# Performance work log

Hardware: AMD Instinct MI355X
Metric: run time of the kernel (lower is better)

Reference implementation:

```python
import jax, jax.numpy as jnp
import numpy as np

B, H, S, DK, DV = 2, 16, 2048, 64, 64

def setup_inputs() -> dict:
    key = jax.random.key(0)
    k1, k2, k3 = jax.random.split(key, 3)
    Q = jax.random.normal(k1, (B, H, S, DK), dtype=jnp.float32)
    K = jax.random.normal(k2, (B, H, S, DK), dtype=jnp.float32)
    V = jax.random.normal(k3, (B, H, S, DV), dtype=jnp.float32)
    mask = jnp.zeros((1, 1, S, S), dtype=jnp.float32)  # additive mask, broadcastable
    return {"Q": Q, "K": K, "V": V, "mask": mask}

def reference(Q, K, V, mask):
    d_k = Q.shape[-1]
    scale = 1.0 / jnp.sqrt(jnp.asarray(d_k, dtype=Q.dtype))
    # [..., q, k] = Q @ K^T / sqrt(d_k) + mask (additive)
    logits = jnp.einsum('bhqd,bhkd->bhqk', Q, K) * scale + mask
    attn = jax.nn.softmax(logits, axis=-1)
    return jnp.einsum('bhqk,bhkv->bhqv', attn, V)
```

## Files before the change

kernel.cpp:

```cpp
#include <hip/hip_runtime.h>


constexpr int Bn = 2, Hn = 16, Sn = 2048, Dn = 64;
constexpr int QB = 128;
constexpr int KVB = 64;
constexpr int NIT = Sn / KVB;
constexpr float SCALE = 0.125f;
constexpr float DEFER_THR = 8.0f;

typedef __attribute__((ext_vector_type(8))) short bf16x8;
typedef __attribute__((ext_vector_type(4))) float f32x4;
typedef __attribute__((ext_vector_type(16))) float f32x16;

union FragU { bf16x8 v; unsigned u[4]; };

__device__ __forceinline__ unsigned cvt_pk(float lo, float hi) {
  unsigned r;
  asm("v_cvt_pk_bf16_f32 %0, %1, %2" : "=v"(r) : "v"(lo), "v"(hi));
  return r;
}

__global__ __launch_bounds__(256, 2) void sdpa_fa3(
    const float* __restrict__ Q, const float* __restrict__ K,
    const float* __restrict__ V, const float* __restrict__ M,
    float* __restrict__ Out) {
  __shared__ unsigned short Kt[2][64 * 64];
  __shared__ unsigned short Vt[2][64 * 64];

  const int tid = threadIdx.x;
  const int lane = tid & 63;
  const int wave = tid >> 6;
  const int l31 = lane & 31;
  const int hi = lane >> 5;
  const int l7 = lane & 7;

  int bid = blockIdx.x;
  bid = (bid & 7) * ((int)gridDim.x >> 3) + (bid >> 3);
  const int head = bid >> 4;
  const int qblk = bid & 15;
  const int qrow = qblk * QB + wave * 32 + l31;

  const float* __restrict__ Qh = Q + (size_t)head * Sn * Dn;
  const float* __restrict__ Kh = K + (size_t)head * Sn * Dn;
  const float* __restrict__ Vh = V + (size_t)head * Sn * Dn;
  float* __restrict__ Oh = Out + (size_t)head * Sn * Dn;
  const float* __restrict__ Mrow = M + (size_t)qrow * Sn;

  FragU qf[4];
#pragma unroll
  for (int kc = 0; kc < 4; ++kc) {
    const float* p = Qh + (size_t)qrow * Dn + kc * 16 + hi * 8;
    f32x4 a = *(const f32x4*)p;
    f32x4 b = *(const f32x4*)(p + 4);
    qf[kc].u[0] = cvt_pk(a[0] * SCALE, a[1] * SCALE);
    qf[kc].u[1] = cvt_pk(a[2] * SCALE, a[3] * SCALE);
    qf[kc].u[2] = cvt_pk(b[0] * SCALE, b[1] * SCALE);
    qf[kc].u[3] = cvt_pk(b[2] * SCALE, b[3] * SCALE);
  }

  f32x16 acc0, acc1;
#pragma unroll
  for (int i = 0; i < 16; ++i) { acc0[i] = 0.f; acc1[i] = 0.f; }
  float m_run = -1e30f, l_run = 0.f;

  const int krow = tid >> 2, kcb = tid & 3;
  const int vk4 = tid >> 4, vcb = tid & 15;

  f32x4 kr[4], vr[4];
  {
    const float* kp = Kh + (size_t)krow * Dn + kcb * 16;
#pragma unroll
    for (int u = 0; u < 4; ++u) kr[u] = *(const f32x4*)(kp + 4 * u);
    const float* vp = Vh + (size_t)(4 * vk4) * Dn + vcb * 4;
#pragma unroll
    for (int r = 0; r < 4; ++r) vr[r] = *(const f32x4*)(vp + (size_t)r * Dn);
#pragma unroll
    for (int b = 0; b < 2; ++b) {
      FragU f;
      f.u[0] = cvt_pk(kr[2 * b][0], kr[2 * b][1]);
      f.u[1] = cvt_pk(kr[2 * b][2], kr[2 * b][3]);
      f.u[2] = cvt_pk(kr[2 * b + 1][0], kr[2 * b + 1][1]);
      f.u[3] = cvt_pk(kr[2 * b + 1][2], kr[2 * b + 1][3]);
      const int pos = (2 * kcb + b) ^ (krow & 7);
      *(bf16x8*)&Kt[0][krow * 64 + pos * 8] = f.v;
    }
#pragma unroll
    for (int j = 0; j < 4; ++j) {
      const int d = 4 * vcb + j;
      unsigned w0 = cvt_pk(vr[0][j], vr[1][j]);
      unsigned w1 = cvt_pk(vr[2][j], vr[3][j]);
      const int pos = (vk4 >> 1) ^ (d & 7);
      unsigned* dst = (unsigned*)&Vt[0][d * 64 + pos * 8 + (vk4 & 1) * 4];
      dst[0] = w0; dst[1] = w1;
    }
  }
  __syncthreads();

  for (int it = 0; it < NIT; ++it) {
    const int kv0 = it * KVB;
    const int cur = it & 1;
    const unsigned short* Kb = Kt[cur];
    const unsigned short* Vb = Vt[cur];

    if (it + 1 < NIT) {
      const float* kp = Kh + (size_t)(kv0 + KVB + krow) * Dn + kcb * 16;
#pragma unroll
      for (int u = 0; u < 4; ++u) kr[u] = *(const f32x4*)(kp + 4 * u);
      const float* vp = Vh + (size_t)(kv0 + KVB + 4 * vk4) * Dn + vcb * 4;
#pragma unroll
      for (int r = 0; r < 4; ++r) vr[r] = *(const f32x4*)(vp + (size_t)r * Dn);
    }

#pragma unroll
    for (int t = 0; t < 2; ++t) {
      f32x4 mk[4];
#pragma unroll
      for (int m = 0; m < 4; ++m)
        mk[m] = *(const f32x4*)(Mrow + kv0 + 32 * t + 8 * m + 4 * hi);

      f32x16 st;
#pragma unroll
      for (int i = 0; i < 16; ++i) st[i] = 0.f;
      __builtin_amdgcn_s_setprio(1);
#pragma unroll
      for (int kc = 0; kc < 4; ++kc) {
        FragU kf;
        kf.v = *(const bf16x8*)&Kb[(32 * t + l31) * 64 + (((2 * kc + hi) ^ l7) * 8)];
        st = __builtin_amdgcn_mfma_f32_32x32x16_bf16(kf.v, qf[kc].v, st, 0, 0, 0);
      }
      __builtin_amdgcn_s_setprio(0);

      float p[16];
#pragma unroll
      for (int m = 0; m < 4; ++m)
#pragma unroll
        for (int e = 0; e < 4; ++e) p[4 * m + e] = st[4 * m + e] + mk[m][e];

      float t8[8];
#pragma unroll
      for (int i = 0; i < 8; ++i) t8[i] = fmaxf(p[2 * i], p[2 * i + 1]);
      float t4a = fmaxf(t8[0], t8[1]), t4b = fmaxf(t8[2], t8[3]);
      float t4c = fmaxf(t8[4], t8[5]), t4d = fmaxf(t8[6], t8[7]);
      float mx = fmaxf(fmaxf(t4a, t4b), fmaxf(t4c, t4d));
      mx = fmaxf(mx, __shfl_xor(mx, 32, 64));

      if (!__all(mx <= m_run + DEFER_THR)) {
        const float mn = fmaxf(m_run, mx);
        const float corr = __expf(m_run - mn);
        m_run = mn;
        l_run *= corr;
#pragma unroll
        for (int i = 0; i < 16; ++i) { acc0[i] *= corr; acc1[i] *= corr; }
      }

      float ps = 0.f;
#pragma unroll
      for (int i = 0; i < 16; ++i) {
        p[i] = __expf(p[i] - m_run);
        ps += p[i];
      }
      ps += __shfl_xor(ps, 32, 64);
      l_run += ps;

      unsigned W[4][2];
#pragma unroll
      for (int m = 0; m < 4; ++m)
#pragma unroll
        for (int s = 0; s < 2; ++s)
          W[m][s] = cvt_pk(p[4 * m + 2 * s], p[4 * m + 2 * s + 1]);

      FragU pf[2];
#pragma unroll
      for (int cc = 0; cc < 2; ++cc)
#pragma unroll
        for (int s = 0; s < 2; ++s) {
          const unsigned a = W[2 * cc][s];
          const unsigned b = W[2 * cc + 1][s];
          const unsigned pa = (unsigned)__shfl_xor((int)a, 32, 64);
          const unsigned pb = (unsigned)__shfl_xor((int)b, 32, 64);
          pf[cc].u[s] = hi ? pb : a;
          pf[cc].u[2 + s] = hi ? b : pa;
        }

      __builtin_amdgcn_s_setprio(1);
#pragma unroll
      for (int cc = 0; cc < 2; ++cc) {
        const int c = 2 * t + cc;
        FragU vf0, vf1;
        vf0.v = *(const bf16x8*)&Vb[(l31) * 64 + (((2 * c + hi) ^ l7) * 8)];
        vf1.v = *(const bf16x8*)&Vb[(32 + l31) * 64 + (((2 * c + hi) ^ l7) * 8)];
        acc0 = __builtin_amdgcn_mfma_f32_32x32x16_bf16(vf0.v, pf[cc].v, acc0, 0, 0, 0);
        acc1 = __builtin_amdgcn_mfma_f32_32x32x16_bf16(vf1.v, pf[cc].v, acc1, 0, 0, 0);
      }
      __builtin_amdgcn_s_setprio(0);
    }

    if (it + 1 < NIT) {
#pragma unroll
      for (int b = 0; b < 2; ++b) {
        FragU f;
        f.u[0] = cvt_pk(kr[2 * b][0], kr[2 * b][1]);
        f.u[1] = cvt_pk(kr[2 * b][2], kr[2 * b][3]);
        f.u[2] = cvt_pk(kr[2 * b + 1][0], kr[2 * b + 1][1]);
        f.u[3] = cvt_pk(kr[2 * b + 1][2], kr[2 * b + 1][3]);
        const int pos = (2 * kcb + b) ^ (krow & 7);
        *(bf16x8*)&Kt[cur ^ 1][krow * 64 + pos * 8] = f.v;
      }
#pragma unroll
      for (int j = 0; j < 4; ++j) {
        const int d = 4 * vcb + j;
        unsigned w0 = cvt_pk(vr[0][j], vr[1][j]);
        unsigned w1 = cvt_pk(vr[2][j], vr[3][j]);
        const int pos = (vk4 >> 1) ^ (d & 7);
        unsigned* dst = (unsigned*)&Vt[cur ^ 1][d * 64 + pos * 8 + (vk4 & 1) * 4];
        dst[0] = w0; dst[1] = w1;
      }
    }
    __syncthreads();
  }

  const float inv = 1.0f / l_run;
#pragma unroll
  for (int m = 0; m < 4; ++m) {
    f32x4 o0, o1;
#pragma unroll
    for (int e = 0; e < 4; ++e) { o0[e] = acc0[4 * m + e] * inv; o1[e] = acc1[4 * m + e] * inv; }
    *(f32x4*)&Oh[(size_t)qrow * Dn + 8 * m + 4 * hi] = o0;
    *(f32x4*)&Oh[(size_t)qrow * Dn + 32 + 8 * m + 4 * hi] = o1;
  }
}

extern "C" void kernel_launch(void* const* d_in, const int* in_sizes, int n_in,
                              void* d_out, int out_size, void* d_ws, size_t ws_size,
                              hipStream_t stream) {
  const float* Q = (const float*)d_in[0];
  const float* K = (const float*)d_in[1];
  const float* V = (const float*)d_in[2];
  const float* M = (const float*)d_in[3];
  float* O = (float*)d_out;
  dim3 grid(Bn * Hn * (Sn / QB));
  sdpa_fa3<<<grid, dim3(256), 0, stream>>>(Q, K, V, M, O);
}
```

Before: 190.7 us.

## Split KV range across two wave groups per block with LDS merge, exp2 softmax

Each block now runs 512 threads, with two groups of four waves each processing half of the KV sequence (split-K style). The partial outputs are merged through LDS at the end using the running max and sum. The tile shrinks to 32 KV rows per iteration. The mask is staged cooperatively into LDS as bf16 pre-scaled by log2e, and the softmax uses raw v_exp_f32 with log2e folded into the Q scale. This is meant to raise parallelism and occupancy and cut the per-lane uncoalesced mask loads. In exchange it doubles the syncthreads count, adds a final LDS reduction, and rounds the mask to bf16, which could lose precision for non-zero masks.

```diff
diff --git a/kernel.cpp b/kernel.cpp
--- a/kernel.cpp
+++ b/kernel.cpp
@@ -3,48 +3,66 @@
 
 constexpr int Bn = 2, Hn = 16, Sn = 2048, Dn = 64;
 constexpr int QB = 128;
-constexpr int KVB = 64;
-constexpr int NIT = Sn / KVB;
-constexpr float SCALE = 0.125f;
+constexpr int KVB = 32;
+constexpr int HALFKV = 1024;
+constexpr int NIT = HALFKV / KVB;
+constexpr float LOG2E = 1.44269504088896f;
+constexpr float QSCALE = 0.125f * LOG2E;
 constexpr float DEFER_THR = 8.0f;
 
 typedef __attribute__((ext_vector_type(8))) short bf16x8;
 typedef __attribute__((ext_vector_type(4))) float f32x4;
 typedef __attribute__((ext_vector_type(16))) float f32x16;
 
-union FragU { bf16x8 v; unsigned u[4]; };
+union FragU { bf16x8 v; unsigned u[4]; unsigned short s[8]; };
+union B64U { unsigned long long q; unsigned short s[4]; };
 
 __device__ __forceinline__ unsigned cvt_pk(float lo, float hi) {
   unsigned r;
   asm("v_cvt_pk_bf16_f32 %0, %1, %2" : "=v"(r) : "v"(lo), "v"(hi));
   return r;
 }
-
-__global__ __launch_bounds__(256, 2) void sdpa_fa3(
+__device__ __forceinline__ float exp2_fast(float x) {
+  float r;
+  asm("v_exp_f32 %0, %1" : "=v"(r) : "v"(x));
+  return r;
+}
+__device__ __forceinline__ float bf2f(unsigned short b) {
+  union { unsigned u; float f; } c;
+  c.u = ((unsigned)b) << 16;
+  return c.f;
+}
+
+__global__ __launch_bounds__(512, 4) void sdpa_fa4(
     const float* __restrict__ Q, const float* __restrict__ K,
     const float* __restrict__ V, const float* __restrict__ M,
     float* __restrict__ Out) {
-  __shared__ unsigned short Kt[2][64 * 64];
-  __shared__ unsigned short Vt[2][64 * 64];
+  __shared__ __align__(16) unsigned short lds[32768];
 
   const int tid = threadIdx.x;
   const int lane = tid & 63;
   const int wave = tid >> 6;
+  const int wq = wave & 3;
+  const int half = tid >> 8;
+  const int htid = tid & 255;
   const int l31 = lane & 31;
   const int hi = lane >> 5;
-  const int l7 = lane & 7;
 
   int bid = blockIdx.x;
   bid = (bid & 7) * ((int)gridDim.x >> 3) + (bid >> 3);
   const int head = bid >> 4;
   const int qblk = bid & 15;
-  const int qrow = qblk * QB + wave * 32 + l31;
+  const int qrow = qblk * QB + wq * 32 + l31;
+  const int kvh = half * HALFKV;
 
   const float* __restrict__ Qh = Q + (size_t)head * Sn * Dn;
   const float* __restrict__ Kh = K + (size_t)head * Sn * Dn;
   const float* __restrict__ Vh = V + (size_t)head * Sn * Dn;
   float* __restrict__ Oh = Out + (size_t)head * Sn * Dn;
-  const float* __restrict__ Mrow = M + (size_t)qrow * Sn;
+
+  unsigned short* Kt = lds + half * 16384;
+  unsigned short* Vt = lds + half * 16384 + 4096;
+  unsigned short* Mt = lds + half * 16384 + 8192;
 
   FragU qf[4];
 #pragma unroll
@@ -52,10 +70,10 @@
     const float* p = Qh + (size_t)qrow * Dn + kc * 16 + hi * 8;
     f32x4 a = *(const f32x4*)p;
     f32x4 b = *(const f32x4*)(p + 4);
-    qf[kc].u[0] = cvt_pk(a[0] * SCALE, a[1] * SCALE);
-    qf[kc].u[1] = cvt_pk(a[2] * SCALE, a[3] * SCALE);
-    qf[kc].u[2] = cvt_pk(b[0] * SCALE, b[1] * SCALE);
-    qf[kc].u[3] = cvt_pk(b[2] * SCALE, b[3] * SCALE);
+    qf[kc].u[0] = cvt_pk(a[0] * QSCALE, a[1] * QSCALE);
+    qf[kc].u[1] = cvt_pk(a[2] * QSCALE, a[3] * QSCALE);
+    qf[kc].u[2] = cvt_pk(b[0] * QSCALE, b[1] * QSCALE);
+    qf[kc].u[3] = cvt_pk(b[2] * QSCALE, b[3] * QSCALE);
   }
 
   f32x16 acc0, acc1;
@@ -63,170 +81,210 @@
   for (int i = 0; i < 16; ++i) { acc0[i] = 0.f; acc1[i] = 0.f; }
   float m_run = -1e30f, l_run = 0.f;
 
-  const int krow = tid >> 2, kcb = tid & 3;
-  const int vk4 = tid >> 4, vcb = tid & 15;
-
-  f32x4 kr[4], vr[4];
+  const int krow = htid >> 3, kcb = htid & 7;
+  const int vd = htid & 63, vkb = htid >> 6;
+  const int mq = htid >> 1, mh = htid & 1;
+
+  f32x4 kr0, kr1;
+  float vrg[8];
+  f32x4 mr[4];
+
   {
-    const float* kp = Kh + (size_t)krow * Dn + kcb * 16;
-#pragma unroll
-    for (int u = 0; u < 4; ++u) kr[u] = *(const f32x4*)(kp + 4 * u);
-    const float* vp = Vh + (size_t)(4 * vk4) * Dn + vcb * 4;
-#pragma unroll
-    for (int r = 0; r < 4; ++r) vr[r] = *(const f32x4*)(vp + (size_t)r * Dn);
-#pragma unroll
-    for (int b = 0; b < 2; ++b) {
+    const float* kp = Kh + (size_t)(kvh + krow) * Dn + kcb * 8;
+    kr0 = *(const f32x4*)kp;
+    kr1 = *(const f32x4*)(kp + 4);
+    const float* vp = Vh + (size_t)(kvh + vkb * 8) * Dn + vd;
+#pragma unroll
+    for (int r = 0; r < 8; ++r) vrg[r] = vp[(size_t)r * Dn];
+    const float* mp = M + (size_t)(qblk * QB + mq) * Sn + kvh + mh * 16;
+#pragma unroll
+    for (int u = 0; u < 4; ++u) mr[u] = *(const f32x4*)(mp + 4 * u);
+
+    FragU f;
+    f.u[0] = cvt_pk(kr0[0], kr0[1]); f.u[1] = cvt_pk(kr0[2], kr0[3]);
+    f.u[2] = cvt_pk(kr1[0], kr1[1]); f.u[3] = cvt_pk(kr1[2], kr1[3]);
+    *(bf16x8*)&Kt[krow * 64 + ((kcb ^ (krow & 7)) * 8)] = f.v;
+    FragU g;
+    g.u[0] = cvt_pk(vrg[0], vrg[1]); g.u[1] = cvt_pk(vrg[2], vrg[3]);
+    g.u[2] = cvt_pk(vrg[4], vrg[5]); g.u[3] = cvt_pk(vrg[6], vrg[7]);
+    *(bf16x8*)&Vt[vd * 32 + ((vkb ^ ((vd >> 2) & 3)) * 8)] = g.v;
+    FragU h0, h1;
+    h0.u[0] = cvt_pk(mr[0][0] * LOG2E, mr[0][1] * LOG2E);
+    h0.u[1] = cvt_pk(mr[0][2] * LOG2E, mr[0][3] * LOG2E);
+    h0.u[2] = cvt_pk(mr[1][0] * LOG2E, mr[1][1] * LOG2E);
+    h0.u[3] = cvt_pk(mr[1][2] * LOG2E, mr[1][3] * LOG2E);
+    h1.u[0] = cvt_pk(mr[2][0] * LOG2E, mr[2][1] * LOG2E);
+    h1.u[1] = cvt_pk(mr[2][2] * LOG2E, mr[2][3] * LOG2E);
+    h1.u[2] = cvt_pk(mr[3][0] * LOG2E, mr[3][1] * LOG2E);
+    h1.u[3] = cvt_pk(mr[3][2] * LOG2E, mr[3][3] * LOG2E);
+    *(bf16x8*)&Mt[mq * 32 + (((mh * 2 + 0) ^ (mq & 3)) * 8)] = h0.v;
+    *(bf16x8*)&Mt[mq * 32 + (((mh * 2 + 1) ^ (mq & 3)) * 8)] = h1.v;
+  }
+  __syncthreads();
+
+  for (int it = 0; it < NIT; ++it) {
+    const int cur = it & 1;
+    const unsigned short* Kb = Kt + cur * 2048;
+    const unsigned short* Vb = Vt + cur * 2048;
+    const unsigned short* Mb = Mt + cur * 4096;
+
+    if (it + 1 < NIT) {
+      const int kv1 = kvh + (it + 1) * KVB;
+      const float* kp = Kh + (size_t)(kv1 + krow) * Dn + kcb * 8;
+      kr0 = *(const f32x4*)kp;
+      kr1 = *(const f32x4*)(kp + 4);
+      const float* vp = Vh + (size_t)(kv1 + vkb * 8) * Dn + vd;
+#pragma unroll
+      for (int r = 0; r < 8; ++r) vrg[r] = vp[(size_t)r * Dn];
+      const float* mp = M + (size_t)(qblk * QB + mq) * Sn + kv1 + mh * 16;
+#pragma unroll
+      for (int u = 0; u < 4; ++u) mr[u] = *(const f32x4*)(mp + 4 * u);
+    }
+
+    f32x16 st;
+#pragma unroll
+    for (int i = 0; i < 16; ++i) st[i] = 0.f;
+    __builtin_amdgcn_s_setprio(1);
+#pragma unroll
+    for (int kc = 0; kc < 4; ++kc) {
+      FragU kf;
+      kf.v = *(const bf16x8*)&Kb[l31 * 64 + (((2 * kc + hi) ^ (l31 & 7)) * 8)];
+      st = __builtin_amdgcn_mfma_f32_32x32x16_bf16(kf.v, qf[kc].v, st, 0, 0, 0);
+    }
+    __builtin_amdgcn_s_setprio(0);
+
+    float p[16];
+#pragma unroll
+    for (int m = 0; m < 4; ++m) {
+      B64U mb;
+      mb.q = *(const unsigned long long*)
+          &Mb[(wq * 32 + l31) * 32 + ((m ^ (l31 & 3)) * 8) + hi * 4];
+#pragma unroll
+      for (int e = 0; e < 4; ++e) p[4 * m + e] = st[4 * m + e] + bf2f(mb.s[e]);
+    }
+
+    float t8[8];
+#pragma unroll
+    for (int i = 0; i < 8; ++i) t8[i] = fmaxf(p[2 * i], p[2 * i + 1]);
+    float t4a = fmaxf(t8[0], t8[1]), t4b = fmaxf(t8[2], t8[3]);
+    float t4c = fmaxf(t8[4], t8[5]), t4d = fmaxf(t8[6], t8[7]);
+    float mx = fmaxf(fmaxf(t4a, t4b), fmaxf(t4c, t4d));
+    mx = fmaxf(mx, __shfl_xor(mx, 32, 64));
+
+    if (!__all(mx <= m_run + DEFER_THR)) {
+      const float mn = fmaxf(m_run, mx);
+      const float corr = exp2_fast(m_run - mn);
+      m_run = mn;
+      l_run *= corr;
+#pragma unroll
+      for (int i = 0; i < 16; ++i) { acc0[i] *= corr; acc1[i] *= corr; }
+    }
+
+    float ps = 0.f;
+#pragma unroll
+    for (int i = 0; i < 16; ++i) {
+      p[i] = exp2_fast(p[i] - m_run);
+      ps += p[i];
+    }
+    ps += __shfl_xor(ps, 32, 64);
+    l_run += ps;
+
+    unsigned W[4][2];
+#pragma unroll
+    for (int m = 0; m < 4; ++m)
+#pragma unroll
+      for (int s = 0; s < 2; ++s)
+        W[m][s] = cvt_pk(p[4 * m + 2 * s], p[4 * m + 2 * s + 1]);
+
+    FragU pf[2];
+#pragma unroll
+    for (int cc = 0; cc < 2; ++cc)
+#pragma unroll
+      for (int s = 0; s < 2; ++s) {
+        const unsigned a = W[2 * cc][s];
+        const unsigned b = W[2 * cc + 1][s];
+        const unsigned pa = (unsigned)__shfl_xor((int)a, 32, 64);
+        const unsigned pb = (unsigned)__shfl_xor((int)b, 32, 64);
+        pf[cc].u[s] = hi ? pb : a;
+        pf[cc].u[2 + s] = hi ? b : pa;
+      }
+
+    __builtin_amdgcn_s_setprio(1);
+#pragma unroll
+    for (int c = 0; c < 2; ++c) {
+      FragU vf0, vf1;
+      vf0.v = *(const bf16x8*)&Vb[l31 * 32 + (((2 * c + hi) ^ ((l31 >> 2) & 3)) * 8)];
+      vf1.v = *(const bf16x8*)&Vb[(32 + l31) * 32 + (((2 * c + hi) ^ ((l31 >> 2) & 3)) * 8)];
+      acc0 = __builtin_amdgcn_mfma_f32_32x32x16_bf16(vf0.v, pf[c].v, acc0, 0, 0, 0);
+      acc1 = __builtin_amdgcn_mfma_f32_32x32x16_bf16(vf1.v, pf[c].v, acc1, 0, 0, 0);
+    }
+    __builtin_amdgcn_s_setprio(0);
+
+    if (it + 1 < NIT) {
+      unsigned short* Kw = Kt + (cur ^ 1) * 2048;
+      unsigned short* Vw = Vt + (cur ^ 1) * 2048;
+      unsigned short* Mw = Mt + (cur ^ 1) * 4096;
       FragU f;
-      f.u[0] = cvt_pk(kr[2 * b][0], kr[2 * b][1]);
-      f.u[1] = cvt_pk(kr[2 * b][2], kr[2 * b][3]);
-      f.u[2] = cvt_pk(kr[2 * b + 1][0], kr[2 * b + 1][1]);
-      f.u[3] = cvt_pk(kr[2 * b + 1][2], kr[2 * b + 1][3]);
-      const int pos = (2 * kcb + b) ^ (krow & 7);
-      *(bf16x8*)&Kt[0][krow * 64 + pos * 8] = f.v;
-    }
-#pragma unroll
-    for (int j = 0; j < 4; ++j) {
-      const int d = 4 * vcb + j;
-      unsigned w0 = cvt_pk(vr[0][j], vr[1][j]);
-      unsigned w1 = cvt_pk(vr[2][j], vr[3][j]);
-      const int pos = (vk4 >> 1) ^ (d & 7);
-      unsigned* dst = (unsigned*)&Vt[0][d * 64 + pos * 8 + (vk4 & 1) * 4];
-      dst[0] = w0; dst[1] = w1;
-    }
+      f.u[0] = cvt_pk(kr0[0], kr0[1]); f.u[1] = cvt_pk(kr0[2], kr0[3]);
+      f.u[2] = cvt_pk(kr1[0], kr1[1]); f.u[3] = cvt_pk(kr1[2], kr1[3]);
+      *(bf16x8*)&Kw[krow * 64 + ((kcb ^ (krow & 7)) * 8)] = f.v;
+      FragU g;
+      g.u[0] = cvt_pk(vrg[0], vrg[1]); g.u[1] = cvt_pk(vrg[2], vrg[3]);
+      g.u[2] = cvt_pk(vrg[4], vrg[5]); g.u[3] = cvt_pk(vrg[6], vrg[7]);
+      *(bf16x8*)&Vw[vd * 32 + ((vkb ^ ((vd >> 2) & 3)) * 8)] = g.v;
+      FragU h0, h1;
+      h0.u[0] = cvt_pk(mr[0][0] * LOG2E, mr[0][1] * LOG2E);
+      h0.u[1] = cvt_pk(mr[0][2] * LOG2E, mr[0][3] * LOG2E);
+      h0.u[2] = cvt_pk(mr[1][0] * LOG2E, mr[1][1] * LOG2E);
+      h0.u[3] = cvt_pk(mr[1][2] * LOG2E, mr[1][3] * LOG2E);
+      h1.u[0] = cvt_pk(mr[2][0] * LOG2E, mr[2][1] * LOG2E);
+      h1.u[1] = cvt_pk(mr[2][2] * LOG2E, mr[2][3] * LOG2E);
+      h1.u[2] = cvt_pk(mr[3][0] * LOG2E, mr[3][1] * LOG2E);
+      h1.u[3] = cvt_pk(mr[3][2] * LOG2E, mr[3][3] * LOG2E);
+      *(bf16x8*)&Mw[mq * 32 + (((mh * 2 + 0) ^ (mq & 3)) * 8)] = h0.v;
+      *(bf16x8*)&Mw[mq * 32 + (((mh * 2 + 1) ^ (mq & 3)) * 8)] = h1.v;
+    }
+    __syncthreads();
+  }
+
+  float* Om = (float*)lds;
+  float* Mm = (float*)lds + 4 * 32 * 68;
+  float* Lm = Mm + 128;
+
+  if (half) {
+    float* base = Om + (wq * 32 + l31) * 68;
+#pragma unroll
+    for (int m = 0; m < 4; ++m) {
+      f32x4 a, b;
+#pragma unroll
+      for (int e = 0; e < 4; ++e) { a[e] = acc0[4 * m + e]; b[e] = acc1[4 * m + e]; }
+      *(f32x4*)(base + 8 * m + 4 * hi) = a;
+      *(f32x4*)(base + 32 + 8 * m + 4 * hi) = b;
+    }
+    if (!hi) { Mm[wq * 32 + l31] = m_run; Lm[wq * 32 + l31] = l_run; }
   }
   __syncthreads();
-
-  for (int it = 0; it < NIT; ++it) {
-    const int kv0 = it * KVB;
-    const int cur = it & 1;
-    const unsigned short* Kb = Kt[cur];
-    const unsigned short* Vb = Vt[cur];
-
-    if (it + 1 < NIT) {
-      const float* kp = Kh + (size_t)(kv0 + KVB + krow) * Dn + kcb * 16;
-#pragma unroll
-      for (int u = 0; u < 4; ++u) kr[u] = *(const f32x4*)(kp + 4 * u);
-      const float* vp = Vh + (size_t)(kv0 + KVB + 4 * vk4) * Dn + vcb * 4;
-#pragma unroll
-      for (int r = 0; r < 4; ++r) vr[r] = *(const f32x4*)(vp + (size_t)r * Dn);
-    }
-
-#pragma unroll
-    for (int t = 0; t < 2; ++t) {
-      f32x4 mk[4];
-#pragma unroll
-      for (int m = 0; m < 4; ++m)
-        mk[m] = *(const f32x4*)(Mrow + kv0 + 32 * t + 8 * m + 4 * hi);
-
-      f32x16 st;
-#pragma unroll
-      for (int i = 0; i < 16; ++i) st[i] = 0.f;
-      __builtin_amdgcn_s_setprio(1);
-#pragma unroll
-      for (int kc = 0; kc < 4; ++kc) {
-        FragU kf;
-        kf.v = *(const bf16x8*)&Kb[(32 * t + l31) * 64 + (((2 * kc + hi) ^ l7) * 8)];
-        st = __builtin_amdgcn_mfma_f32_32x32x16_bf16(kf.v, qf[kc].v, st, 0, 0, 0);
+  if (!half) {
+    const float m2 = Mm[wq * 32 + l31];
+    const float l2 = Lm[wq * 32 + l31];
+    const float mm = fmaxf(m_run, m2);
+    const float e1 = exp2_fast(m_run - mm);
+    const float e2 = exp2_fast(m2 - mm);
+    const float inv = 1.0f / (l_run * e1 + l2 * e2);
+    const float* base = Om + (wq * 32 + l31) * 68;
+#pragma unroll
+    for (int m = 0; m < 4; ++m) {
+      f32x4 o2a = *(const f32x4*)(base + 8 * m + 4 * hi);
+      f32x4 o2b = *(const f32x4*)(base + 32 + 8 * m + 4 * hi);
+      f32x4 oa, ob;
+#pragma unroll
+      for (int e = 0; e < 4; ++e) {
+        oa[e] = (acc0[4 * m + e] * e1 + o2a[e] * e2) * inv;
+        ob[e] = (acc1[4 * m + e] * e1 + o2b[e] * e2) * inv;
       }
-      __builtin_amdgcn_s_setprio(0);
-
-      float p[16];
-#pragma unroll
-      for (int m = 0; m < 4; ++m)
-#pragma unroll
-        for (int e = 0; e < 4; ++e) p[4 * m + e] = st[4 * m + e] + mk[m][e];
-
-      float t8[8];
-#pragma unroll
-      for (int i = 0; i < 8; ++i) t8[i] = fmaxf(p[2 * i], p[2 * i + 1]);
-      float t4a = fmaxf(t8[0], t8[1]), t4b = fmaxf(t8[2], t8[3]);
-      float t4c = fmaxf(t8[4], t8[5]), t4d = fmaxf(t8[6], t8[7]);
-      float mx = fmaxf(fmaxf(t4a, t4b), fmaxf(t4c, t4d));
-      mx = fmaxf(mx, __shfl_xor(mx, 32, 64));
-
-      if (!__all(mx <= m_run + DEFER_THR)) {
-        const float mn = fmaxf(m_run, mx);
-        const float corr = __expf(m_run - mn);
-        m_run = mn;
-        l_run *= corr;
-#pragma unroll
-        for (int i = 0; i < 16; ++i) { acc0[i] *= corr; acc1[i] *= corr; }
-      }
-
-      float ps = 0.f;
-#pragma unroll
-      for (int i = 0; i < 16; ++i) {
-        p[i] = __expf(p[i] - m_run);
-        ps += p[i];
-      }
-      ps += __shfl_xor(ps, 32, 64);
-      l_run += ps;
-
-      unsigned W[4][2];
-#pragma unroll
-      for (int m = 0; m < 4; ++m)
-#pragma unroll
-        for (int s = 0; s < 2; ++s)
-          W[m][s] = cvt_pk(p[4 * m + 2 * s], p[4 * m + 2 * s + 1]);
-
-      FragU pf[2];
-#pragma unroll
-      for (int cc = 0; cc < 2; ++cc)
-#pragma unroll
-        for (int s = 0; s < 2; ++s) {
-          const unsigned a = W[2 * cc][s];
-          const unsigned b = W[2 * cc + 1][s];
-          const unsigned pa = (unsigned)__shfl_xor((int)a, 32, 64);
-          const unsigned pb = (unsigned)__shfl_xor((int)b, 32, 64);
-          pf[cc].u[s] = hi ? pb : a;
-          pf[cc].u[2 + s] = hi ? b : pa;
-        }
-
-      __builtin_amdgcn_s_setprio(1);
-#pragma unroll
-      for (int cc = 0; cc < 2; ++cc) {
-        const int c = 2 * t + cc;
-        FragU vf0, vf1;
-        vf0.v = *(const bf16x8*)&Vb[(l31) * 64 + (((2 * c + hi) ^ l7) * 8)];
-        vf1.v = *(const bf16x8*)&Vb[(32 + l31) * 64 + (((2 * c + hi) ^ l7) * 8)];
-        acc0 = __builtin_amdgcn_mfma_f32_32x32x16_bf16(vf0.v, pf[cc].v, acc0, 0, 0, 0);
-        acc1 = __builtin_amdgcn_mfma_f32_32x32x16_bf16(vf1.v, pf[cc].v, acc1, 0, 0, 0);
-      }
-      __builtin_amdgcn_s_setprio(0);
-    }
-
-    if (it + 1 < NIT) {
-#pragma unroll
-      for (int b = 0; b < 2; ++b) {
-        FragU f;
-        f.u[0] = cvt_pk(kr[2 * b][0], kr[2 * b][1]);
-        f.u[1] = cvt_pk(kr[2 * b][2], kr[2 * b][3]);
-        f.u[2] = cvt_pk(kr[2 * b + 1][0], kr[2 * b + 1][1]);
-        f.u[3] = cvt_pk(kr[2 * b + 1][2], kr[2 * b + 1][3]);
-        const int pos = (2 * kcb + b) ^ (krow & 7);
-        *(bf16x8*)&Kt[cur ^ 1][krow * 64 + pos * 8] = f.v;
-      }
-#pragma unroll
-      for (int j = 0; j < 4; ++j) {
-        const int d = 4 * vcb + j;
-        unsigned w0 = cvt_pk(vr[0][j], vr[1][j]);
-        unsigned w1 = cvt_pk(vr[2][j], vr[3][j]);
-        const int pos = (vk4 >> 1) ^ (d & 7);
-        unsigned* dst = (unsigned*)&Vt[cur ^ 1][d * 64 + pos * 8 + (vk4 & 1) * 4];
-        dst[0] = w0; dst[1] = w1;
-      }
-    }
-    __syncthreads();
-  }
-
-  const float inv = 1.0f / l_run;
-#pragma unroll
-  for (int m = 0; m < 4; ++m) {
-    f32x4 o0, o1;
-#pragma unroll
-    for (int e = 0; e < 4; ++e) { o0[e] = acc0[4 * m + e] * inv; o1[e] = acc1[4 * m + e] * inv; }
-    *(f32x4*)&Oh[(size_t)qrow * Dn + 8 * m + 4 * hi] = o0;
-    *(f32x4*)&Oh[(size_t)qrow * Dn + 32 + 8 * m + 4 * hi] = o1;
+      *(f32x4*)&Oh[(size_t)qrow * Dn + 8 * m + 4 * hi] = oa;
+      *(f32x4*)&Oh[(size_t)qrow * Dn + 32 + 8 * m + 4 * hi] = ob;
+    }
   }
 }
 
@@ -239,5 +297,5 @@
   const float* M = (const float*)d_in[3];
   float* O = (float*)d_out;
   dim3 grid(Bn * Hn * (Sn / QB));
-  sdpa_fa3<<<grid, dim3(256), 0, stream>>>(Q, K, V, M, O);
-}
+  sdpa_fa4<<<grid, dim3(512), 0, stream>>>(Q, K, V, M, O);
+}
```

Result: faster. 186.0 us (-2.5%).
